# Kernel optimization log

Hardware: AMD Instinct MI355X
Metric: run time of the kernel (lower is better)

Reference implementation:

```python
import jax, jax.numpy as jnp
import numpy as np

B, C, H, W = 8, 256, 64, 64


def setup_inputs() -> dict:
    key = jax.random.key(0)
    ks = jax.random.split(key, 9)
    s = 1.0 / np.sqrt(C)  # conv2d default init scale
    return {
        "foreground": jax.random.normal(ks[0], (B, C, H, W), jnp.float32),
        "background": jax.random.normal(ks[1], (B, C, H, W), jnp.float32),
        "mask": jax.random.uniform(ks[2], (B, C, H, W), jnp.float32),
        "Wq": jax.random.normal(ks[3], (C, C), jnp.float32) * s,
        "bq": jnp.zeros((C,), jnp.float32),
        "Wk": jax.random.normal(ks[4], (C, C), jnp.float32) * s,
        "bk": jnp.zeros((C,), jnp.float32),
        "Wv": jax.random.normal(ks[5], (C, C), jnp.float32) * s,
        "bv": jnp.zeros((C,), jnp.float32),
        "gamma": jnp.ones((1,), jnp.float32),
    }


def _conv1x1(x, Wt, b):
    # 1x1 conv == per-pixel channel matmul; x: [B,C,H,W], Wt: [Cout,Cin]
    return jnp.einsum('bchw,oc->bohw', x, Wt) + b[None, :, None, None]


def reference(foreground, background, mask, Wq, bq, Wk, bk, Wv, bv, gamma):
    b, c, h, w = foreground.shape
    hw = h * w
    # mask is already at feature resolution (interpolate would be identity)
    q = _conv1x1(foreground, Wq, bq).reshape(b, c, hw)   # [B,C,HW]
    k = _conv1x1(background, Wk, bk).reshape(b, c, hw)   # [B,C,HW]
    # bmm(q, k^T): channel-channel correlation [B,C,C]
    corr = jnp.einsum('bci,bdi->bcd', q, k)
    m_r = mask.reshape(b, c, hw)                          # [B,C,HW]
    # bmm(corr, m_r): mask-modulated scores [B,C,HW]
    scores = jnp.einsum('bcd,bdi->bci', corr, m_r)
    energy = jax.nn.softmax(scores, axis=-1)
    v = _conv1x1(foreground, Wv, bv).reshape(b, c, hw)
    attended = (energy * v).reshape(b, c, h, w)
    out = foreground * mask + gamma[0] * (1.0 - mask) * attended
    return out
```

## Files before the change

kernel.cpp:

```cpp
#include <hip/hip_runtime.h>
#include <math.h>

#define B_    8
#define C_    256
#define HW_   4096
#define CHW_  ((long)C_ * HW_)

#define BKT   32
#define LDH   40
#define KS    16
#define KCH   (HW_ / KS)
#define NCH   (C_ / BKT)

typedef __attribute__((ext_vector_type(8))) short bf16x8;
typedef __attribute__((ext_vector_type(4))) float f32x4;
#define MFMA_BF16(a, b, c) __builtin_amdgcn_mfma_f32_16x16x32_bf16((a), (b), (c), 0, 0, 0)

union frag_u { uint4 u4; bf16x8 bf; };

#define GLOAD_LDS16(src, dst)                                              \
    __builtin_amdgcn_global_load_lds(                                      \
        (const __attribute__((address_space(1))) void*)(src),              \
        (__attribute__((address_space(3))) void*)(dst), 16, 0, 0)

__device__ __forceinline__ void cvt_hl4(const float4 f, uint* h, uint* l) {
    uint u0 = __float_as_uint(f.x), u1 = __float_as_uint(f.y),
         u2 = __float_as_uint(f.z), u3 = __float_as_uint(f.w);
    uint h0 = (u0 + 0x8000u) & 0xFFFF0000u, h1 = (u1 + 0x8000u) & 0xFFFF0000u,
         h2 = (u2 + 0x8000u) & 0xFFFF0000u, h3 = (u3 + 0x8000u) & 0xFFFF0000u;
    h[0] = (h0 >> 16) | h1;
    h[1] = (h2 >> 16) | h3;
    float l0 = f.x - __uint_as_float(h0), l1 = f.y - __uint_as_float(h1),
          l2 = f.z - __uint_as_float(h2), l3 = f.w - __uint_as_float(h3);
    uint a0 = __float_as_uint(l0) & 0xFFFF0000u, a1 = __float_as_uint(l1) & 0xFFFF0000u,
         a2 = __float_as_uint(l2) & 0xFFFF0000u, a3 = __float_as_uint(l3) & 0xFFFF0000u;
    l[0] = (a0 >> 16) | a1;
    l[1] = (a2 >> 16) | a3;
}
__device__ __forceinline__ void cvt_h4(const float4 f, uint* h) {
    uint u0 = __float_as_uint(f.x), u1 = __float_as_uint(f.y),
         u2 = __float_as_uint(f.z), u3 = __float_as_uint(f.w);
    uint h0 = (u0 + 0x8000u) & 0xFFFF0000u, h1 = (u1 + 0x8000u) & 0xFFFF0000u,
         h2 = (u2 + 0x8000u) & 0xFFFF0000u, h3 = (u3 + 0x8000u) & 0xFFFF0000u;
    h[0] = (h0 >> 16) | h1;
    h[1] = (h2 >> 16) | h3;
}

__device__ __forceinline__ void cvt2_hl(float a, float b2, uint* h, uint* l) {
    uint ua = __float_as_uint(a), ub = __float_as_uint(b2);
    uint ha = (ua + 0x8000u) & 0xFFFF0000u, hb = (ub + 0x8000u) & 0xFFFF0000u;
    *h = (ha >> 16) | hb;
    float la = a - __uint_as_float(ha), lb = b2 - __uint_as_float(hb);
    *l = ((__float_as_uint(la) & 0xFFFF0000u) >> 16) | (__float_as_uint(lb) & 0xFFFF0000u);
}
__device__ __forceinline__ uint cvt2_h(float a, float b2) {
    uint ha = (__float_as_uint(a) + 0x8000u) & 0xFFFF0000u;
    uint hb = (__float_as_uint(b2) + 0x8000u) & 0xFFFF0000u;
    return (ha >> 16) | hb;
}

__global__ __launch_bounds__(256) void conv_w(
    const float* __restrict__ Wv, ushort* __restrict__ Wvh)
{
    const int i = (blockIdx.x * 256 + threadIdx.x) * 4;
    float4 v = *reinterpret_cast<const float4*>(&Wv[i]);
    uint h[2];
    cvt_h4(v, h);
    *reinterpret_cast<uint2*>(&Wvh[i]) = make_uint2(h[0], h[1]);
}

__global__ __launch_bounds__(256) void transpose_cvt(
    const float* __restrict__ mask, const float* __restrict__ fg,
    ushort* __restrict__ mTh, ushort* __restrict__ mTl, ushort* __restrict__ fTh)
{
    __shared__ float Ms[64][65];
    __shared__ float Fs[64][65];

    const int b  = blockIdx.z;
    const int c0 = blockIdx.y * 64;
    const int i0 = blockIdx.x * 64;
    const int t  = threadIdx.x;

    const int lr = t >> 2;
    const int lc = (t & 3) * 16;
    const float* mp = mask + (long)b * CHW_ + (long)(c0 + lr) * HW_ + i0 + lc;
    const float* fp = fg   + (long)b * CHW_ + (long)(c0 + lr) * HW_ + i0 + lc;
    #pragma unroll
    for (int j = 0; j < 16; j += 4) {
        *reinterpret_cast<float4*>(&Ms[lr][lc + j]) = *reinterpret_cast<const float4*>(mp + j);
        *reinterpret_cast<float4*>(&Fs[lr][lc + j]) = *reinterpret_cast<const float4*>(fp + j);
    }
    __syncthreads();

    const int oi = t >> 2;
    const int oc = (t & 3) * 16;
    uint hm[8], lm[8], hf[8];
    #pragma unroll
    for (int j = 0; j < 8; ++j) {
        const float m0v = Ms[oc + 2 * j][oi], m1v = Ms[oc + 2 * j + 1][oi];
        cvt2_hl(m0v, m1v, &hm[j], &lm[j]);
        hf[j] = cvt2_h(Fs[oc + 2 * j][oi], Fs[oc + 2 * j + 1][oi]);
    }
    const long ro = ((long)b * HW_ + i0 + oi) * C_ + c0 + oc;
    *reinterpret_cast<uint4*>(&mTh[ro])     = make_uint4(hm[0], hm[1], hm[2], hm[3]);
    *reinterpret_cast<uint4*>(&mTh[ro + 8]) = make_uint4(hm[4], hm[5], hm[6], hm[7]);
    *reinterpret_cast<uint4*>(&mTl[ro])     = make_uint4(lm[0], lm[1], lm[2], lm[3]);
    *reinterpret_cast<uint4*>(&mTl[ro + 8]) = make_uint4(lm[4], lm[5], lm[6], lm[7]);
    *reinterpret_cast<uint4*>(&fTh[ro])     = make_uint4(hf[0], hf[1], hf[2], hf[3]);
    *reinterpret_cast<uint4*>(&fTh[ro + 8]) = make_uint4(hf[4], hf[5], hf[6], hf[7]);
}

__global__ __launch_bounds__(256, 3) void gemm_nt_mfma(
    const float* __restrict__ F, const float* __restrict__ G,
    float* __restrict__ part,
    float* __restrict__ fsum, float* __restrict__ gsum)
{
    __shared__ ushort Ah[128 * LDH], Al[128 * LDH], Bh[128 * LDH], Bl[128 * LDH];

    const int z  = blockIdx.z;
    const int b  = z >> 4;
    const int ks = z & (KS - 1);
    const int c0 = blockIdx.y * 128;
    const int d0 = blockIdx.x * 128;
    const float* Fb = F + (long)b * CHW_ + (long)ks * KCH;
    const float* Gb = G + (long)b * CHW_ + (long)ks * KCH;
    const bool doF = (blockIdx.x == 0);
    const bool doG = (blockIdx.y == 0);

    const int t    = threadIdx.x;
    const int srow = t & 127;
    const int skf  = (t >> 7) * 16;
    const int lane = t & 63, w = t >> 6;
    const int col  = lane & 15, quad = lane >> 4;
    const int wm   = (w >> 1) * 64, wn = (w & 1) * 64;

    f32x4 acc[4][4] = {};
    float rsF = 0.0f, rsG = 0.0f;

    for (int kt = 0; kt < KCH; kt += BKT) {
        {
            const float* s = &Fb[(long)(c0 + srow) * HW_ + kt + skf];
            float4 v0 = *reinterpret_cast<const float4*>(s);
            float4 v1 = *reinterpret_cast<const float4*>(s + 4);
            float4 v2 = *reinterpret_cast<const float4*>(s + 8);
            float4 v3 = *reinterpret_cast<const float4*>(s + 12);
            if (doF) {
                rsF += (v0.x + v0.y + v0.z + v0.w) + (v1.x + v1.y + v1.z + v1.w)
                     + (v2.x + v2.y + v2.z + v2.w) + (v3.x + v3.y + v3.z + v3.w);
            }
            uint h[4], l[4];
            cvt_hl4(v0, h + 0, l + 0);
            cvt_hl4(v1, h + 2, l + 2);
            *reinterpret_cast<uint4*>(&Ah[srow * LDH + skf]) = make_uint4(h[0], h[1], h[2], h[3]);
            *reinterpret_cast<uint4*>(&Al[srow * LDH + skf]) = make_uint4(l[0], l[1], l[2], l[3]);
            cvt_hl4(v2, h + 0, l + 0);
            cvt_hl4(v3, h + 2, l + 2);
            *reinterpret_cast<uint4*>(&Ah[srow * LDH + skf + 8]) = make_uint4(h[0], h[1], h[2], h[3]);
            *reinterpret_cast<uint4*>(&Al[srow * LDH + skf + 8]) = make_uint4(l[0], l[1], l[2], l[3]);
        }
        {
            const float* s = &Gb[(long)(d0 + srow) * HW_ + kt + skf];
            float4 v0 = *reinterpret_cast<const float4*>(s);
            float4 v1 = *reinterpret_cast<const float4*>(s + 4);
            float4 v2 = *reinterpret_cast<const float4*>(s + 8);
            float4 v3 = *reinterpret_cast<const float4*>(s + 12);
            if (doG) {
                rsG += (v0.x + v0.y + v0.z + v0.w) + (v1.x + v1.y + v1.z + v1.w)
                     + (v2.x + v2.y + v2.z + v2.w) + (v3.x + v3.y + v3.z + v3.w);
            }
            uint h[4], l[4];
            cvt_hl4(v0, h + 0, l + 0);
            cvt_hl4(v1, h + 2, l + 2);
            *reinterpret_cast<uint4*>(&Bh[srow * LDH + skf]) = make_uint4(h[0], h[1], h[2], h[3]);
            *reinterpret_cast<uint4*>(&Bl[srow * LDH + skf]) = make_uint4(l[0], l[1], l[2], l[3]);
            cvt_hl4(v2, h + 0, l + 0);
            cvt_hl4(v3, h + 2, l + 2);
            *reinterpret_cast<uint4*>(&Bh[srow * LDH + skf + 8]) = make_uint4(h[0], h[1], h[2], h[3]);
            *reinterpret_cast<uint4*>(&Bl[srow * LDH + skf + 8]) = make_uint4(l[0], l[1], l[2], l[3]);
        }
        __syncthreads();

        bf16x8 bfh[4], bfl[4];
        #pragma unroll
        for (int tj = 0; tj < 4; ++tj) {
            const int r = (wn + tj * 16 + col) * LDH + quad * 8;
            bfh[tj] = *reinterpret_cast<const bf16x8*>(&Bh[r]);
            bfl[tj] = *reinterpret_cast<const bf16x8*>(&Bl[r]);
        }
        #pragma unroll
        for (int ti = 0; ti < 4; ++ti) {
            const int r = (wm + ti * 16 + col) * LDH + quad * 8;
            bf16x8 afh = *reinterpret_cast<const bf16x8*>(&Ah[r]);
            bf16x8 afl = *reinterpret_cast<const bf16x8*>(&Al[r]);
            #pragma unroll
            for (int tj = 0; tj < 4; ++tj) {
                acc[ti][tj] = MFMA_BF16(afh, bfh[tj], acc[ti][tj]);
                acc[ti][tj] = MFMA_BF16(afh, bfl[tj], acc[ti][tj]);
                acc[ti][tj] = MFMA_BF16(afl, bfh[tj], acc[ti][tj]);
            }
        }
        __syncthreads();
    }

    if (doF) atomicAdd(&fsum[b * C_ + c0 + srow], rsF);
    if (doG) atomicAdd(&gsum[b * C_ + d0 + srow], rsG);

    float* P = part + (long)z * C_ * C_;
    #pragma unroll
    for (int ti = 0; ti < 4; ++ti) {
        const int m = c0 + wm + ti * 16 + quad * 4;
        #pragma unroll
        for (int tj = 0; tj < 4; ++tj) {
            const int n = d0 + wn + tj * 16 + col;
            #pragma unroll
            for (int r = 0; r < 4; ++r)
                P[(long)(m + r) * C_ + n] = acc[ti][tj][r];
        }
    }
}

__global__ __launch_bounds__(256, 3) void gemm_stats_mfma(
    const ushort* __restrict__ corrh, const ushort* __restrict__ corrl,
    const ushort* __restrict__ mTh,   const ushort* __restrict__ mTl,
    float* __restrict__ pmax, float* __restrict__ psum)
{
    __shared__ __align__(16) ushort Bst[2][2][4096];
    __shared__ float pm[2][128], ps[2][128];

    const int b  = blockIdx.z;
    const int m0 = blockIdx.y * 128;
    const int n0 = blockIdx.x * 128;
    const ushort* Ahb = corrh + (long)b * C_ * C_;
    const ushort* Alb = corrl + (long)b * C_ * C_;
    const ushort* Bhb = mTh + (long)b * HW_ * C_;
    const ushort* Blb = mTl + (long)b * HW_ * C_;

    const int t    = threadIdx.x;
    const int lane = t & 63, w = t >> 6;
    const int col  = lane & 15, quad = lane >> 4;
    const int wm   = (w >> 1) * 64, wn = (w & 1) * 64;
    const int qsw  = (lane & 3) ^ ((lane >> 3) & 3);
    const int srw  = lane >> 2;

    const ushort* gsrcs[2] = { Bhb, Blb };

#define STAGE_S(buf, kk) do {                                              \
    _Pragma("unroll")                                                      \
    for (int a = 0; a < 2; ++a) {                                          \
        _Pragma("unroll")                                                  \
        for (int gg = 0; gg < 2; ++gg) {                                   \
            const int g = w * 2 + gg;                                      \
            const ushort* src = gsrcs[a]                                   \
                + (long)(n0 + g * 16 + srw) * C_ + (kk) + qsw * 8;         \
            GLOAD_LDS16(src, &Bst[buf][a][g * 512]);                       \
        }                                                                  \
    }                                                                      \
} while (0)

    int boff[4];
    #pragma unroll
    for (int tj = 0; tj < 4; ++tj) {
        const int rowB = wn + tj * 16 + col;
        boff[tj] = rowB * 64 + ((quad ^ ((rowB >> 1) & 3)) << 4);
    }

    f32x4 acc[4][4] = {};

    STAGE_S(0, 0);
    __syncthreads();

    int cur = 0;
    #pragma unroll 1
    for (int kc = 0; kc < NCH; ++kc) {
        const int kt = kc * BKT;

        bf16x8 ah[4], al[4];
        #pragma unroll
        for (int ti = 0; ti < 4; ++ti) {
            const long oa = (long)(m0 + wm + ti * 16 + col) * C_ + kt + quad * 8;
            ah[ti] = *reinterpret_cast<const bf16x8*>(&Ahb[oa]);
            al[ti] = *reinterpret_cast<const bf16x8*>(&Alb[oa]);
        }

        if (kc + 1 < NCH) STAGE_S(cur ^ 1, kt + BKT);

        const char* base = (const char*)&Bst[cur][0][0];
        bf16x8 bh[4], bl[4];
        #pragma unroll
        for (int tj = 0; tj < 4; ++tj) {
            bh[tj] = *reinterpret_cast<const bf16x8*>(base + boff[tj]);
            bl[tj] = *reinterpret_cast<const bf16x8*>(base + 8192 + boff[tj]);
        }

        #pragma unroll
        for (int tj = 0; tj < 4; ++tj) {
            #pragma unroll
            for (int ti = 0; ti < 4; ++ti) {
                acc[ti][tj] = MFMA_BF16(ah[ti], bh[tj], acc[ti][tj]);
                acc[ti][tj] = MFMA_BF16(ah[ti], bl[tj], acc[ti][tj]);
                acc[ti][tj] = MFMA_BF16(al[ti], bh[tj], acc[ti][tj]);
            }
        }
        __syncthreads();
        cur ^= 1;
    }
#undef STAGE_S

    #pragma unroll
    for (int ti = 0; ti < 4; ++ti) {
        #pragma unroll
        for (int r = 0; r < 4; ++r) {
            float mx = fmaxf(fmaxf(acc[ti][0][r], acc[ti][1][r]),
                             fmaxf(acc[ti][2][r], acc[ti][3][r]));
            mx = fmaxf(mx, __shfl_xor(mx, 1));
            mx = fmaxf(mx, __shfl_xor(mx, 2));
            mx = fmaxf(mx, __shfl_xor(mx, 4));
            mx = fmaxf(mx, __shfl_xor(mx, 8));
            float se2 = __expf(acc[ti][0][r] - mx) + __expf(acc[ti][1][r] - mx)
                      + __expf(acc[ti][2][r] - mx) + __expf(acc[ti][3][r] - mx);
            se2 += __shfl_xor(se2, 1);
            se2 += __shfl_xor(se2, 2);
            se2 += __shfl_xor(se2, 4);
            se2 += __shfl_xor(se2, 8);
            if (col == 0) {
                const int rb = wm + ti * 16 + quad * 4 + r;
                pm[w & 1][rb] = mx;
                ps[w & 1][rb] = se2;
            }
        }
    }
    __syncthreads();
    if (t < 128) {
        const float a0 = pm[0][t], a1 = pm[1][t];
        const float gm = fmaxf(a0, a1);
        const float gs = ps[0][t] * __expf(a0 - gm) + ps[1][t] * __expf(a1 - gm);
        const long rowg = (long)b * C_ + m0 + t;
        pmax[rowg * 32 + blockIdx.x] = gm;
        psum[rowg * 32 + blockIdx.x] = gs;
    }
}

__global__ __launch_bounds__(256, 2) void gemm_fused_final(
    const ushort* __restrict__ corrh, const ushort* __restrict__ corrl,
    const ushort* __restrict__ Wvh,
    const ushort* __restrict__ mTh,   const ushort* __restrict__ mTl,
    const ushort* __restrict__ fTh,
    const float* __restrict__ mask,   const float* __restrict__ fg,
    const float* __restrict__ pmax,   const float* __restrict__ psum,
    const float* __restrict__ bv,     const float* __restrict__ gamma,
    float* __restrict__ out)
{
    __shared__ __align__(16) ushort Bst[2][3][4096];
    __shared__ float sm[128], si[128];

    const int b  = blockIdx.z;
    const int m0 = blockIdx.y * 128;
    const int n0 = blockIdx.x * 128;
    const ushort* Ahb = corrh + (long)b * C_ * C_;
    const ushort* Alb = corrl + (long)b * C_ * C_;
    const ushort* Bhb = mTh + (long)b * HW_ * C_;
    const ushort* Blb = mTl + (long)b * HW_ * C_;
    const ushort* Bfb = fTh + (long)b * HW_ * C_;

    const int t    = threadIdx.x;
    const int lane = t & 63, w = t >> 6;
    const int col  = lane & 15, quad = lane >> 4;
    const int wm   = (w >> 1) * 64, wn = (w & 1) * 64;
    const int qsw  = (lane & 3) ^ ((lane >> 3) & 3);
    const int srw  = lane >> 2;

    const ushort* gsrcs[3] = { Bhb, Blb, Bfb };

#define STAGE_F(buf, kk) do {                                              \
    _Pragma("unroll")                                                      \
    for (int a = 0; a < 3; ++a) {                                          \
        _Pragma("unroll")                                                  \
        for (int gg = 0; gg < 2; ++gg) {                                   \
            const int g = w * 2 + gg;                                      \
            const ushort* src = gsrcs[a]                                   \
                + (long)(n0 + g * 16 + srw) * C_ + (kk) + qsw * 8;         \
            GLOAD_LDS16(src, &Bst[buf][a][g * 512]);                       \
        }                                                                  \
    }                                                                      \
} while (0)

    if (t < 128) {
        const long rowg = (long)b * C_ + m0 + t;
        const float* pmr = pmax + rowg * 32;
        const float* psr = psum + rowg * 32;
        float gm = -INFINITY;
        #pragma unroll
        for (int i = 0; i < 32; ++i) gm = fmaxf(gm, pmr[i]);
        float gs = 0.0f;
        #pragma unroll
        for (int i = 0; i < 32; ++i) gs += psr[i] * __expf(pmr[i] - gm);
        sm[t] = gm;
        si[t] = 1.0f / gs;
    }

    int boff[4];
    #pragma unroll
    for (int tj = 0; tj < 4; ++tj) {
        const int rowB = wn + tj * 16 + col;
        boff[tj] = rowB * 64 + ((quad ^ ((rowB >> 1) & 3)) << 4);
    }

    f32x4 acc_s[4][4] = {};
    f32x4 acc_v[4][4] = {};

    STAGE_F(0, 0);
    __syncthreads();

    int cur = 0;
    #pragma unroll 1
    for (int kc = 0; kc < NCH; ++kc) {
        const int kt = kc * BKT;

        bf16x8 ah[4], al[4], aw[4];
        #pragma unroll
        for (int ti = 0; ti < 4; ++ti) {
            const long oa = (long)(m0 + wm + ti * 16 + col) * C_ + kt + quad * 8;
            ah[ti] = *reinterpret_cast<const bf16x8*>(&Ahb[oa]);
            al[ti] = *reinterpret_cast<const bf16x8*>(&Alb[oa]);
            aw[ti] = *reinterpret_cast<const bf16x8*>(&Wvh[oa]);
        }

        if (kc + 1 < NCH) STAGE_F(cur ^ 1, kt + BKT);

        const char* base = (const char*)&Bst[cur][0][0];
        bf16x8 bh[4], bl[4], bf[4];
        #pragma unroll
        for (int tj = 0; tj < 4; ++tj) {
            bh[tj] = *reinterpret_cast<const bf16x8*>(base + boff[tj]);
            bl[tj] = *reinterpret_cast<const bf16x8*>(base + 8192 + boff[tj]);
            bf[tj] = *reinterpret_cast<const bf16x8*>(base + 16384 + boff[tj]);
        }

        #pragma unroll
        for (int tj = 0; tj < 4; ++tj) {
            #pragma unroll
            for (int ti = 0; ti < 4; ++ti) {
                acc_s[ti][tj] = MFMA_BF16(ah[ti], bh[tj], acc_s[ti][tj]);
                acc_s[ti][tj] = MFMA_BF16(ah[ti], bl[tj], acc_s[ti][tj]);
                acc_s[ti][tj] = MFMA_BF16(al[ti], bh[tj], acc_s[ti][tj]);
                acc_v[ti][tj] = MFMA_BF16(aw[ti], bf[tj], acc_v[ti][tj]);
            }
        }
        __syncthreads();
        cur ^= 1;
    }
#undef STAGE_F

    const float g = gamma[0];
    #pragma unroll
    for (int ti = 0; ti < 4; ++ti) {
        #pragma unroll
        for (int r = 0; r < 4; ++r) {
            const int lrow = wm + ti * 16 + quad * 4 + r;
            const float mx  = sm[lrow];
            const float inv = si[lrow] * g;
            #pragma unroll
            for (int tj = 0; tj < 4; ++tj)
                acc_s[ti][tj][r] = __expf(acc_s[ti][tj][r] - mx) * inv;
        }
    }

    #pragma unroll
    for (int ti = 0; ti < 4; ++ti) {
        const int m = m0 + wm + ti * 16 + quad * 4;
        #pragma unroll
        for (int r = 0; r < 4; ++r) {
            const float bvm = bv[m + r];
            #pragma unroll
            for (int tj = 0; tj < 4; ++tj) {
                const int n = n0 + wn + tj * 16 + col;
                const long e = (long)b * CHW_ + (long)(m + r) * HW_ + n;
                const float f  = fg[e];
                const float mk = mask[e];
                const float vv = acc_v[ti][tj][r] + bvm;
                out[e] = f * mk + (1.0f - mk) * acc_s[ti][tj][r] * vv;
            }
        }
    }
}

__global__ __launch_bounds__(256) void reduce_part(
    const float* __restrict__ part, float* __restrict__ S1)
{
    const long idx = (long)blockIdx.x * 256 + threadIdx.x;
    const int  b   = (int)(idx >> 16);
    const long e   = idx & 65535;
    const float* p = part + ((long)b * KS) * 65536 + e;
    float s = 0.0f;
    #pragma unroll
    for (int ks = 0; ks < KS; ++ks) s += p[(long)ks * 65536];
    S1[idx] = s;
}

#define BK64 16
#define LDT64 68
__global__ __launch_bounds__(256) void gemm_nt64(
    const float* __restrict__ S1, const float* __restrict__ Wk,
    float* __restrict__ T)
{
    __shared__ float As[BK64][LDT64];
    __shared__ float Bs[BK64][LDT64];
    const int r0 = blockIdx.y * 64;
    const int d0 = blockIdx.x * 64;
    const int t   = threadIdx.x;
    const int tx  = t & 15, ty = t >> 4;
    const int tx4 = tx * 4, ty4 = ty * 4;
    const int am  = t >> 2, ak4 = (t & 3) * 4;

    float acc[4][4] = {};
    for (int k0 = 0; k0 < C_; k0 += BK64) {
        float4 av = *reinterpret_cast<const float4*>(&S1[(long)(r0 + am) * C_ + k0 + ak4]);
        float4 bw = *reinterpret_cast<const float4*>(&Wk[(long)(d0 + am) * C_ + k0 + ak4]);
        As[ak4+0][am]=av.x; As[ak4+1][am]=av.y; As[ak4+2][am]=av.z; As[ak4+3][am]=av.w;
        Bs[ak4+0][am]=bw.x; Bs[ak4+1][am]=bw.y; Bs[ak4+2][am]=bw.z; Bs[ak4+3][am]=bw.w;
        __syncthreads();
        #pragma unroll
        for (int kk = 0; kk < BK64; ++kk) {
            float4 a = *reinterpret_cast<const float4*>(&As[kk][ty4]);
            float4 x = *reinterpret_cast<const float4*>(&Bs[kk][tx4]);
            const float ar[4] = {a.x,a.y,a.z,a.w};
            const float xr[4] = {x.x,x.y,x.z,x.w};
            #pragma unroll
            for (int r = 0; r < 4; ++r)
                #pragma unroll
                for (int s = 0; s < 4; ++s)
                    acc[r][s] = fmaf(ar[r], xr[s], acc[r][s]);
        }
        __syncthreads();
    }
    #pragma unroll
    for (int r = 0; r < 4; ++r) {
        float4 o; o.x=acc[r][0]; o.y=acc[r][1]; o.z=acc[r][2]; o.w=acc[r][3];
        *reinterpret_cast<float4*>(&T[(long)(r0 + ty4 + r) * C_ + d0 + tx4]) = o;
    }
}

__global__ __launch_bounds__(256) void gemm_nn64_rank1(
    const float* __restrict__ Wq, const float* __restrict__ T,
    const float* __restrict__ Wk, const float* __restrict__ bk,
    const float* __restrict__ bq,
    const float* __restrict__ fsum, const float* __restrict__ gsum,
    ushort* __restrict__ corrh, ushort* __restrict__ corrl)
{
    __shared__ float As[BK64][LDT64];
    __shared__ float Bs[BK64][LDT64];
    __shared__ float u_s[64], wh_s[64];
    const int b  = blockIdx.z;
    const int m0 = blockIdx.y * 64;
    const int n0 = blockIdx.x * 64;
    const float* Tb = T + (long)b * C_ * C_;

    const int t   = threadIdx.x;
    const int tx  = t & 15, ty = t >> 4;
    const int tx4 = tx * 4, ty4 = ty * 4;
    const int am  = t >> 2, ak4 = (t & 3) * 4;
    const int xk  = ty,     xn4 = tx4;

    if (t < 64) {
        const float* wrow = Wq + (long)(m0 + t) * C_;
        const float* s = fsum + b * C_;
        float a = 0.0f;
        for (int e2 = 0; e2 < C_; ++e2) a = fmaf(wrow[e2], s[e2], a);
        u_s[t] = a;
    } else if (t < 128) {
        const int d = n0 + (t - 64);
        const float* wrow = Wk + (long)d * C_;
        const float* s = gsum + b * C_;
        float a = 0.0f;
        for (int e2 = 0; e2 < C_; ++e2) a = fmaf(wrow[e2], s[e2], a);
        wh_s[t - 64] = a + (float)HW_ * bk[d];
    }

    float acc[4][4] = {};
    for (int k0 = 0; k0 < C_; k0 += BK64) {
        float4 av = *reinterpret_cast<const float4*>(&Wq[(long)(m0 + am) * C_ + k0 + ak4]);
        float4 xv = *reinterpret_cast<const float4*>(&Tb[(long)(k0 + xk) * C_ + n0 + xn4]);
        As[ak4+0][am]=av.x; As[ak4+1][am]=av.y; As[ak4+2][am]=av.z; As[ak4+3][am]=av.w;
        *reinterpret_cast<float4*>(&Bs[xk][xn4]) = xv;
        __syncthreads();
        #pragma unroll
        for (int kk = 0; kk < BK64; ++kk) {
            float4 a = *reinterpret_cast<const float4*>(&As[kk][ty4]);
            float4 x = *reinterpret_cast<const float4*>(&Bs[kk][tx4]);
            const float ar[4] = {a.x,a.y,a.z,a.w};
            const float xr[4] = {x.x,x.y,x.z,x.w};
            #pragma unroll
            for (int r = 0; r < 4; ++r)
                #pragma unroll
                for (int s = 0; s < 4; ++s)
                    acc[r][s] = fmaf(ar[r], xr[s], acc[r][s]);
        }
        __syncthreads();
    }

    float4 bkv = *reinterpret_cast<const float4*>(&bk[n0 + tx4]);
    float4 whv = make_float4(wh_s[tx4], wh_s[tx4+1], wh_s[tx4+2], wh_s[tx4+3]);
    #pragma unroll
    for (int r = 0; r < 4; ++r) {
        const int m = m0 + ty4 + r;
        const float um = u_s[ty4 + r];
        const float bm = bq[m];
        float4 o;
        o.x = acc[r][0] + um*bkv.x + bm*whv.x;
        o.y = acc[r][1] + um*bkv.y + bm*whv.y;
        o.z = acc[r][2] + um*bkv.z + bm*whv.z;
        o.w = acc[r][3] + um*bkv.w + bm*whv.w;
        uint h[2], l[2];
        cvt_hl4(o, h, l);
        const long e = (long)b * C_ * C_ + (long)m * C_ + n0 + tx4;
        *reinterpret_cast<uint2*>(&corrh[e]) = make_uint2(h[0], h[1]);
        *reinterpret_cast<uint2*>(&corrl[e]) = make_uint2(l[0], l[1]);
    }
}

extern "C" void kernel_launch(void* const* d_in, const int* in_sizes, int n_in,
                              void* d_out, int out_size, void* d_ws, size_t ws_size,
                              hipStream_t stream)
{
    const float* fg    = (const float*)d_in[0];
    const float* bg    = (const float*)d_in[1];
    const float* mask  = (const float*)d_in[2];
    const float* Wq    = (const float*)d_in[3];
    const float* bq    = (const float*)d_in[4];
    const float* Wk    = (const float*)d_in[5];
    const float* bk    = (const float*)d_in[6];
    const float* Wv    = (const float*)d_in[7];
    const float* bv    = (const float*)d_in[8];
    const float* gamma = (const float*)d_in[9];
    float* out = (float*)d_out;

    char* ws = (char*)d_ws;
    float*  part   = (float*)(ws);
    float*  S1     = (float*)(ws + 33554432);
    float*  T      = (float*)(ws + 35651584);
    ushort* corrh  = (ushort*)(ws + 37748736);
    ushort* corrl  = (ushort*)(ws + 38797312);
    ushort* Wvh    = (ushort*)(ws + 39845888);
    float*  fsum   = (float*)(ws + 39976960);
    float*  gsum   = (float*)(ws + 39985152);
    float*  pmax   = (float*)(ws + 39993344);
    float*  psum   = (float*)(ws + 40255488);
    ushort* mTh    = (ushort*)(ws);
    ushort* mTl    = (ushort*)(ws + 16777216);
    ushort* fTh    = (ushort*)(ws + 40517632);

    const dim3 blk(256);

    hipMemsetAsync(fsum, 0, 16384, stream);

    conv_w<<<dim3(64), blk, 0, stream>>>(Wv, Wvh);

    gemm_nt_mfma<<<dim3(2, 2, B_ * KS), blk, 0, stream>>>(fg, bg, part, fsum, gsum);
    reduce_part<<<dim3(B_ * C_ * C_ / 256), blk, 0, stream>>>(part, S1);

    transpose_cvt<<<dim3(HW_ / 64, C_ / 64, B_), blk, 0, stream>>>(
        mask, fg, mTh, mTl, fTh);

    gemm_nt64<<<dim3(C_ / 64, B_ * C_ / 64), blk, 0, stream>>>(S1, Wk, T);
    gemm_nn64_rank1<<<dim3(4, 4, B_), blk, 0, stream>>>(
        Wq, T, Wk, bk, bq, fsum, gsum, corrh, corrl);

    gemm_stats_mfma<<<dim3(HW_ / 128, C_ / 128, B_), blk, 0, stream>>>(
        corrh, corrl, mTh, mTl, pmax, psum);

    gemm_fused_final<<<dim3(HW_ / 128, C_ / 128, B_), blk, 0, stream>>>(
        corrh, corrl, Wvh, mTh, mTl, fTh, mask, fg, pmax, psum, bv, gamma, out);
}
```

Measured before the change: 297.8 us.

## Halve N-tile in stats/final GEMMs, stage epilogues through LDS for coalesced stores

```diff
diff --git a/kernel.cpp b/kernel.cpp
--- a/kernel.cpp
+++ b/kernel.cpp
@@ -11,6 +11,7 @@
 #define KS    16
 #define KCH   (HW_ / KS)
 #define NCH   (C_ / BKT)
+#define NPB   64
 
 typedef __attribute__((ext_vector_type(8))) short bf16x8;
 typedef __attribute__((ext_vector_type(4))) float f32x4;
@@ -115,7 +116,9 @@
     float* __restrict__ part,
     float* __restrict__ fsum, float* __restrict__ gsum)
 {
-    __shared__ ushort Ah[128 * LDH], Al[128 * LDH], Bh[128 * LDH], Bl[128 * LDH];
+    __shared__ __align__(16) ushort SMEM[4][128 * LDH];
+    ushort* Ah = SMEM[0]; ushort* Al = SMEM[1];
+    ushort* Bh = SMEM[2]; ushort* Bl = SMEM[3];
 
     const int z  = blockIdx.z;
     const int b  = z >> 4;
@@ -205,31 +208,43 @@
     if (doF) atomicAdd(&fsum[b * C_ + c0 + srow], rsF);
     if (doG) atomicAdd(&gsum[b * C_ + d0 + srow], rsG);
 
+    float* xch = (float*)&SMEM[0][0];
     float* P = part + (long)z * C_ * C_;
-    #pragma unroll
+    const int pr = t >> 3, pu = t & 7;
+    const int mmb = c0 + ((pr & 16) ? 64 : 0) + (pr & 15);
+    #pragma unroll 1
     for (int ti = 0; ti < 4; ++ti) {
-        const int m = c0 + wm + ti * 16 + quad * 4;
+        __syncthreads();
         #pragma unroll
         for (int tj = 0; tj < 4; ++tj) {
-            const int n = d0 + wn + tj * 16 + col;
+            const int lc = wn + tj * 16 + col;
             #pragma unroll
-            for (int r = 0; r < 4; ++r)
-                P[(long)(m + r) * C_ + n] = acc[ti][tj][r];
-        }
-    }
-}
-
-__global__ __launch_bounds__(256, 3) void gemm_stats_mfma(
+            for (int r = 0; r < 4; ++r) {
+                const int lr = (w >> 1) * 16 + quad * 4 + r;
+                xch[lr * 132 + lc] = acc[ti][tj][r];
+            }
+        }
+        __syncthreads();
+        const int mm = mmb + ti * 16;
+        float* dst = &P[(long)mm * C_ + d0 + pu * 16];
+        const float* srcx = &xch[pr * 132 + pu * 16];
+        #pragma unroll
+        for (int j = 0; j < 16; j += 4)
+            *reinterpret_cast<float4*>(dst + j) = *reinterpret_cast<const float4*>(srcx + j);
+    }
+}
+
+__global__ __launch_bounds__(256, 4) void gemm_stats_mfma(
     const ushort* __restrict__ corrh, const ushort* __restrict__ corrl,
     const ushort* __restrict__ mTh,   const ushort* __restrict__ mTl,
     float* __restrict__ pmax, float* __restrict__ psum)
 {
-    __shared__ __align__(16) ushort Bst[2][2][4096];
+    __shared__ __align__(16) ushort Bst[2][2][2048];
     __shared__ float pm[2][128], ps[2][128];
 
     const int b  = blockIdx.z;
     const int m0 = blockIdx.y * 128;
-    const int n0 = blockIdx.x * 128;
+    const int n0 = blockIdx.x * 64;
     const ushort* Ahb = corrh + (long)b * C_ * C_;
     const ushort* Alb = corrl + (long)b * C_ * C_;
     const ushort* Bhb = mTh + (long)b * HW_ * C_;
@@ -238,7 +253,7 @@
     const int t    = threadIdx.x;
     const int lane = t & 63, w = t >> 6;
     const int col  = lane & 15, quad = lane >> 4;
-    const int wm   = (w >> 1) * 64, wn = (w & 1) * 64;
+    const int wm   = (w >> 1) * 64, wn = (w & 1) * 32;
     const int qsw  = (lane & 3) ^ ((lane >> 3) & 3);
     const int srw  = lane >> 2;
 
@@ -247,24 +262,20 @@
 #define STAGE_S(buf, kk) do {                                              \
     _Pragma("unroll")                                                      \
     for (int a = 0; a < 2; ++a) {                                          \
-        _Pragma("unroll")                                                  \
-        for (int gg = 0; gg < 2; ++gg) {                                   \
-            const int g = w * 2 + gg;                                      \
-            const ushort* src = gsrcs[a]                                   \
-                + (long)(n0 + g * 16 + srw) * C_ + (kk) + qsw * 8;         \
-            GLOAD_LDS16(src, &Bst[buf][a][g * 512]);                       \
-        }                                                                  \
+        const ushort* src = gsrcs[a]                                       \
+            + (long)(n0 + w * 16 + srw) * C_ + (kk) + qsw * 8;             \
+        GLOAD_LDS16(src, &Bst[buf][a][w * 512]);                           \
     }                                                                      \
 } while (0)
 
-    int boff[4];
-    #pragma unroll
-    for (int tj = 0; tj < 4; ++tj) {
+    int boff[2];
+    #pragma unroll
+    for (int tj = 0; tj < 2; ++tj) {
         const int rowB = wn + tj * 16 + col;
         boff[tj] = rowB * 64 + ((quad ^ ((rowB >> 1) & 3)) << 4);
     }
 
-    f32x4 acc[4][4] = {};
+    f32x4 acc[4][2] = {};
 
     STAGE_S(0, 0);
     __syncthreads();
@@ -285,15 +296,15 @@
         if (kc + 1 < NCH) STAGE_S(cur ^ 1, kt + BKT);
 
         const char* base = (const char*)&Bst[cur][0][0];
-        bf16x8 bh[4], bl[4];
-        #pragma unroll
-        for (int tj = 0; tj < 4; ++tj) {
+        bf16x8 bh[2], bl[2];
+        #pragma unroll
+        for (int tj = 0; tj < 2; ++tj) {
             bh[tj] = *reinterpret_cast<const bf16x8*>(base + boff[tj]);
-            bl[tj] = *reinterpret_cast<const bf16x8*>(base + 8192 + boff[tj]);
-        }
-
-        #pragma unroll
-        for (int tj = 0; tj < 4; ++tj) {
+            bl[tj] = *reinterpret_cast<const bf16x8*>(base + 4096 + boff[tj]);
+        }
+
+        #pragma unroll
+        for (int tj = 0; tj < 2; ++tj) {
             #pragma unroll
             for (int ti = 0; ti < 4; ++ti) {
                 acc[ti][tj] = MFMA_BF16(ah[ti], bh[tj], acc[ti][tj]);
@@ -310,14 +321,12 @@
     for (int ti = 0; ti < 4; ++ti) {
         #pragma unroll
         for (int r = 0; r < 4; ++r) {
-            float mx = fmaxf(fmaxf(acc[ti][0][r], acc[ti][1][r]),
-                             fmaxf(acc[ti][2][r], acc[ti][3][r]));
+            float mx = fmaxf(acc[ti][0][r], acc[ti][1][r]);
             mx = fmaxf(mx, __shfl_xor(mx, 1));
             mx = fmaxf(mx, __shfl_xor(mx, 2));
             mx = fmaxf(mx, __shfl_xor(mx, 4));
             mx = fmaxf(mx, __shfl_xor(mx, 8));
-            float se2 = __expf(acc[ti][0][r] - mx) + __expf(acc[ti][1][r] - mx)
-                      + __expf(acc[ti][2][r] - mx) + __expf(acc[ti][3][r] - mx);
+            float se2 = __expf(acc[ti][0][r] - mx) + __expf(acc[ti][1][r] - mx);
             se2 += __shfl_xor(se2, 1);
             se2 += __shfl_xor(se2, 2);
             se2 += __shfl_xor(se2, 4);
@@ -335,12 +344,12 @@
         const float gm = fmaxf(a0, a1);
         const float gs = ps[0][t] * __expf(a0 - gm) + ps[1][t] * __expf(a1 - gm);
         const long rowg = (long)b * C_ + m0 + t;
-        pmax[rowg * 32 + blockIdx.x] = gm;
-        psum[rowg * 32 + blockIdx.x] = gs;
-    }
-}
-
-__global__ __launch_bounds__(256, 2) void gemm_fused_final(
+        pmax[rowg * NPB + blockIdx.x] = gm;
+        psum[rowg * NPB + blockIdx.x] = gs;
+    }
+}
+
+__global__ __launch_bounds__(256, 3) void gemm_fused_final(
     const ushort* __restrict__ corrh, const ushort* __restrict__ corrl,
     const ushort* __restrict__ Wvh,
     const ushort* __restrict__ mTh,   const ushort* __restrict__ mTl,
@@ -350,12 +359,12 @@
     const float* __restrict__ bv,     const float* __restrict__ gamma,
     float* __restrict__ out)
 {
-    __shared__ __align__(16) ushort Bst[2][3][4096];
+    __shared__ __align__(16) ushort Bst[2][3][2048];
     __shared__ float sm[128], si[128];
 
     const int b  = blockIdx.z;
     const int m0 = blockIdx.y * 128;
-    const int n0 = blockIdx.x * 128;
+    const int n0 = blockIdx.x * 64;
     const ushort* Ahb = corrh + (long)b * C_ * C_;
     const ushort* Alb = corrl + (long)b * C_ * C_;
     const ushort* Bhb = mTh + (long)b * HW_ * C_;
@@ -365,7 +374,7 @@
     const int t    = threadIdx.x;
     const int lane = t & 63, w = t >> 6;
     const int col  = lane & 15, quad = lane >> 4;
-    const int wm   = (w >> 1) * 64, wn = (w & 1) * 64;
+    const int wm   = (w >> 1) * 64, wn = (w & 1) * 32;
     const int qsw  = (lane & 3) ^ ((lane >> 3) & 3);
     const int srw  = lane >> 2;
 
@@ -374,39 +383,35 @@
 #define STAGE_F(buf, kk) do {                                              \
     _Pragma("unroll")                                                      \
     for (int a = 0; a < 3; ++a) {                                          \
-        _Pragma("unroll")                                                  \
-        for (int gg = 0; gg < 2; ++gg) {                                   \
-            const int g = w * 2 + gg;                                      \
-            const ushort* src = gsrcs[a]                                   \
-                + (long)(n0 + g * 16 + srw) * C_ + (kk) + qsw * 8;         \
-            GLOAD_LDS16(src, &Bst[buf][a][g * 512]);                       \
-        }                                                                  \
+        const ushort* src = gsrcs[a]                                       \
+            + (long)(n0 + w * 16 + srw) * C_ + (kk) + qsw * 8;             \
+        GLOAD_LDS16(src, &Bst[buf][a][w * 512]);                           \
     }                                                                      \
 } while (0)
 
     if (t < 128) {
         const long rowg = (long)b * C_ + m0 + t;
-        const float* pmr = pmax + rowg * 32;
-        const float* psr = psum + rowg * 32;
+        const float* pmr = pmax + rowg * NPB;
+        const float* psr = psum + rowg * NPB;
         float gm = -INFINITY;
         #pragma unroll
-        for (int i = 0; i < 32; ++i) gm = fmaxf(gm, pmr[i]);
+        for (int i = 0; i < NPB; ++i) gm = fmaxf(gm, pmr[i]);
         float gs = 0.0f;
         #pragma unroll
-        for (int i = 0; i < 32; ++i) gs += psr[i] * __expf(pmr[i] - gm);
+        for (int i = 0; i < NPB; ++i) gs += psr[i] * __expf(pmr[i] - gm);
         sm[t] = gm;
         si[t] = 1.0f / gs;
     }
 
-    int boff[4];
-    #pragma unroll
-    for (int tj = 0; tj < 4; ++tj) {
+    int boff[2];
+    #pragma unroll
+    for (int tj = 0; tj < 2; ++tj) {
         const int rowB = wn + tj * 16 + col;
         boff[tj] = rowB * 64 + ((quad ^ ((rowB >> 1) & 3)) << 4);
     }
 
-    f32x4 acc_s[4][4] = {};
-    f32x4 acc_v[4][4] = {};
+    f32x4 acc_s[4][2] = {};
+    f32x4 acc_v[4][2] = {};
 
     STAGE_F(0, 0);
     __syncthreads();
@@ -428,16 +433,16 @@
         if (kc + 1 < NCH) STAGE_F(cur ^ 1, kt + BKT);
 
         const char* base = (const char*)&Bst[cur][0][0];
-        bf16x8 bh[4], bl[4], bf[4];
-        #pragma unroll
-        for (int tj = 0; tj < 4; ++tj) {
+        bf16x8 bh[2], bl[2], bf[2];
+        #pragma unroll
+        for (int tj = 0; tj < 2; ++tj) {
             bh[tj] = *reinterpret_cast<const bf16x8*>(base + boff[tj]);
-            bl[tj] = *reinterpret_cast<const bf16x8*>(base + 8192 + boff[tj]);
-            bf[tj] = *reinterpret_cast<const bf16x8*>(base + 16384 + boff[tj]);
-        }
-
-        #pragma unroll
-        for (int tj = 0; tj < 4; ++tj) {
+            bl[tj] = *reinterpret_cast<const bf16x8*>(base + 4096 + boff[tj]);
+            bf[tj] = *reinterpret_cast<const bf16x8*>(base + 8192 + boff[tj]);
+        }
+
+        #pragma unroll
+        for (int tj = 0; tj < 2; ++tj) {
             #pragma unroll
             for (int ti = 0; ti < 4; ++ti) {
                 acc_s[ti][tj] = MFMA_BF16(ah[ti], bh[tj], acc_s[ti][tj]);
@@ -452,34 +457,42 @@
 #undef STAGE_F
 
     const float g = gamma[0];
-    #pragma unroll
+    float* xch = (float*)&Bst[0][0][0];
+    const int pr = t >> 3, pu = t & 7;
+    const int mmb = m0 + ((pr & 16) ? 64 : 0) + (pr & 15);
+
+    #pragma unroll 1
     for (int ti = 0; ti < 4; ++ti) {
+        __syncthreads();
         #pragma unroll
         for (int r = 0; r < 4; ++r) {
             const int lrow = wm + ti * 16 + quad * 4 + r;
             const float mx  = sm[lrow];
             const float inv = si[lrow] * g;
+            const float bvm = bv[m0 + lrow];
+            const int lr = (w >> 1) * 16 + quad * 4 + r;
             #pragma unroll
-            for (int tj = 0; tj < 4; ++tj)
-                acc_s[ti][tj][r] = __expf(acc_s[ti][tj][r] - mx) * inv;
-        }
-    }
-
-    #pragma unroll
-    for (int ti = 0; ti < 4; ++ti) {
-        const int m = m0 + wm + ti * 16 + quad * 4;
-        #pragma unroll
-        for (int r = 0; r < 4; ++r) {
-            const float bvm = bv[m + r];
-            #pragma unroll
-            for (int tj = 0; tj < 4; ++tj) {
-                const int n = n0 + wn + tj * 16 + col;
-                const long e = (long)b * CHW_ + (long)(m + r) * HW_ + n;
-                const float f  = fg[e];
-                const float mk = mask[e];
+            for (int tj = 0; tj < 2; ++tj) {
+                const float p  = __expf(acc_s[ti][tj][r] - mx) * inv;
                 const float vv = acc_v[ti][tj][r] + bvm;
-                out[e] = f * mk + (1.0f - mk) * acc_s[ti][tj][r] * vv;
-            }
+                xch[lr * 68 + wn + tj * 16 + col] = p * vv;
+            }
+        }
+        __syncthreads();
+        const int mm = mmb + ti * 16;
+        const long e0 = (long)b * CHW_ + (long)mm * HW_ + n0 + pu * 8;
+        const float* srcx = &xch[pr * 68 + pu * 8];
+        #pragma unroll
+        for (int j = 0; j < 8; j += 4) {
+            float4 y = *reinterpret_cast<const float4*>(srcx + j);
+            float4 f = *reinterpret_cast<const float4*>(&fg[e0 + j]);
+            float4 k = *reinterpret_cast<const float4*>(&mask[e0 + j]);
+            float4 o;
+            o.x = f.x * k.x + (1.0f - k.x) * y.x;
+            o.y = f.y * k.y + (1.0f - k.y) * y.y;
+            o.z = f.z * k.z + (1.0f - k.z) * y.z;
+            o.w = f.w * k.w + (1.0f - k.w) * y.w;
+            *reinterpret_cast<float4*>(&out[e0 + j]) = o;
         }
     }
 }
@@ -487,14 +500,17 @@
 __global__ __launch_bounds__(256) void reduce_part(
     const float* __restrict__ part, float* __restrict__ S1)
 {
-    const long idx = (long)blockIdx.x * 256 + threadIdx.x;
-    const int  b   = (int)(idx >> 16);
-    const long e   = idx & 65535;
+    const long i4 = ((long)blockIdx.x * 256 + threadIdx.x) * 4;
+    const int  b  = (int)(i4 >> 16);
+    const long e  = i4 & 65535;
     const float* p = part + ((long)b * KS) * 65536 + e;
-    float s = 0.0f;
-    #pragma unroll
-    for (int ks = 0; ks < KS; ++ks) s += p[(long)ks * 65536];
-    S1[idx] = s;
+    float4 s = make_float4(0.f, 0.f, 0.f, 0.f);
+    #pragma unroll
+    for (int ks = 0; ks < KS; ++ks) {
+        float4 v = *reinterpret_cast<const float4*>(&p[(long)ks * 65536]);
+        s.x += v.x; s.y += v.y; s.z += v.z; s.w += v.w;
+    }
+    *reinterpret_cast<float4*>(&S1[i4]) = s;
 }
 
 #define BK64 16
@@ -643,8 +659,8 @@
     ushort* Wvh    = (ushort*)(ws + 39845888);
     float*  fsum   = (float*)(ws + 39976960);
     float*  gsum   = (float*)(ws + 39985152);
-    float*  pmax   = (float*)(ws + 39993344);
-    float*  psum   = (float*)(ws + 40255488);
+    float*  pmax   = (float*)(ws + 33554432);
+    float*  psum   = (float*)(ws + 34078720);
     ushort* mTh    = (ushort*)(ws);
     ushort* mTl    = (ushort*)(ws + 16777216);
     ushort* fTh    = (ushort*)(ws + 40517632);
@@ -656,7 +672,7 @@
     conv_w<<<dim3(64), blk, 0, stream>>>(Wv, Wvh);
 
     gemm_nt_mfma<<<dim3(2, 2, B_ * KS), blk, 0, stream>>>(fg, bg, part, fsum, gsum);
-    reduce_part<<<dim3(B_ * C_ * C_ / 256), blk, 0, stream>>>(part, S1);
+    reduce_part<<<dim3(B_ * C_ * C_ / 1024), blk, 0, stream>>>(part, S1);
 
     transpose_cvt<<<dim3(HW_ / 64, C_ / 64, B_), blk, 0, stream>>>(
         mask, fg, mTh, mTl, fTh);
@@ -665,9 +681,9 @@
     gemm_nn64_rank1<<<dim3(4, 4, B_), blk, 0, stream>>>(
         Wq, T, Wk, bk, bq, fsum, gsum, corrh, corrl);
 
-    gemm_stats_mfma<<<dim3(HW_ / 128, C_ / 128, B_), blk, 0, stream>>>(
+    gemm_stats_mfma<<<dim3(HW_ / 64, C_ / 128, B_), blk, 0, stream>>>(
         corrh, corrl, mTh, mTl, pmax, psum);
 
-    gemm_fused_final<<<dim3(HW_ / 128, C_ / 128, B_), blk, 0, stream>>>(
+    gemm_fused_final<<<dim3(HW_ / 64, C_ / 128, B_), blk, 0, stream>>>(
         corrh, corrl, Wvh, mTh, mTl, fTh, mask, fg, pmax, psum, bv, gamma, out);
 }
```

After: 479.3 us. 1.61x slower.
